# Optimization experiments

Hardware: AMD Instinct MI355X
Metric: run time of the kernel (lower is better)

The kernel has to match this reference:

```python
import jax, jax.numpy as jnp
import numpy as np

B, T, V = 32, 64, 30000
EMB, H, E, A = 512, 512, 256, 256


def setup_inputs() -> dict:
    key = jax.random.key(0)
    ks = jax.random.split(key, 16)
    s = lambda k, shape, fan: jax.random.normal(k, shape, jnp.float32) / np.sqrt(fan)
    return {
        "encoder_out": jax.random.normal(ks[0], (B, E), jnp.float32),
        "captions": jax.random.randint(ks[1], (B, T), 0, V),
        # attention params
        "We": s(ks[2], (A, E), E), "be": jnp.zeros((A,), jnp.float32),
        "Wd": s(ks[3], (A, H), H), "bd": jnp.zeros((A,), jnp.float32),
        "Wf": s(ks[4], (1, A), A), "bf": jnp.zeros((1,), jnp.float32),
        # embedding table
        "emb_table": s(ks[5], (V, EMB), 1.0),
        # LSTMCell params (PyTorch gate order i,f,g,o)
        "W_ih": s(ks[6], (4 * H, EMB + E), EMB + E),
        "W_hh": s(ks[7], (4 * H, H), H),
        "b_ih": jnp.zeros((4 * H,), jnp.float32),
        "b_hh": jnp.zeros((4 * H,), jnp.float32),
        # output projection
        "W_fc": s(ks[8], (V, H), H), "b_fc": jnp.zeros((V,), jnp.float32),
    }


def reference(encoder_out, captions, We, be, Wd, bd, Wf, bf, emb_table,
              W_ih, W_hh, b_ih, b_hh, W_fc, b_fc):
    # dropout layers are identity (eval mode)
    emb = emb_table[captions]                      # [B, T, EMB]
    att1 = encoder_out @ We.T + be                 # [B, A]  (encoder term, loop-invariant)

    def step(carry, e_t):
        h, c = carry
        # additive attention over a length-1 sequence -> alpha == 1
        att2 = h @ Wd.T + bd                       # [B, A]
        att = jnp.tanh(att1 + att2) @ Wf.T + bf    # [B, 1]
        alpha = jax.nn.softmax(att, axis=1)        # ones, kept for faithfulness
        context = encoder_out * alpha              # [B, E]
        x = jnp.concatenate([e_t, context], axis=1)  # [B, EMB+E]
        gates = x @ W_ih.T + b_ih + h @ W_hh.T + b_hh  # [B, 4H]
        i, f, g, o = jnp.split(gates, 4, axis=1)
        c_new = jax.nn.sigmoid(f) * c + jax.nn.sigmoid(i) * jnp.tanh(g)
        h_new = jax.nn.sigmoid(o) * jnp.tanh(c_new)
        out_t = h_new @ W_fc.T + b_fc              # [B, V]
        return (h_new, c_new), out_t

    h0 = jnp.zeros((encoder_out.shape[0], H), encoder_out.dtype)
    c0 = jnp.zeros_like(h0)
    _, outs = jax.lax.scan(step, (h0, c0), jnp.swapaxes(emb, 0, 1))  # [T, B, V]
    return jnp.swapaxes(outs, 0, 1)                                  # [B, T, V]
```

## Files before the change

### kernel.cpp

```cpp
#include <hip/hip_runtime.h>
#include <hip/hip_bf16.h>


#define BATCH 32
#define TT 64
#define VV 30000
#define HH 512
#define G4 2048
#define KX 768
#define RNN_WG 16
#define CONS_WG 240
#define NTILE 235

typedef __bf16 bf16x8 __attribute__((ext_vector_type(8)));
typedef float f32x4 __attribute__((ext_vector_type(4)));
typedef unsigned long long u64;

#define MFMA(a, b, c) __builtin_amdgcn_mfma_f32_16x16x32_bf16((a), (b), (c), 0, 0, 0)

__device__ __forceinline__ float sigf(float x) {
    return 1.0f / (1.0f + __expf(-x));
}
__device__ __forceinline__ float tanh_fast(float x) {
    return 1.0f - 2.0f / (__expf(2.0f * x) + 1.0f);
}
__device__ __forceinline__ bf16x8 cvt8(const float* __restrict__ p) {
    const f32x4 a = *(const f32x4*)p;
    const f32x4 b = *(const f32x4*)(p + 4);
    bf16x8 r;
    r[0] = (__bf16)a[0]; r[1] = (__bf16)a[1]; r[2] = (__bf16)a[2]; r[3] = (__bf16)a[3];
    r[4] = (__bf16)b[0]; r[5] = (__bf16)b[1]; r[6] = (__bf16)b[2]; r[7] = (__bf16)b[3];
    return r;
}

__global__ __launch_bounds__(256) void pre_kernel(
    const float* __restrict__ enc, const int* __restrict__ captions,
    const float* __restrict__ emb, const float* __restrict__ Wih,
    const float* __restrict__ bih, const float* __restrict__ bhh,
    float* __restrict__ pre) {
    __shared__ __bf16 aT[128 * 32];
    __shared__ __bf16 bT[128 * 32];
    __shared__ int capm[128];

    const int tid = threadIdx.x;
    const int nt = blockIdx.x;
    const int mt = blockIdx.y;

    if (tid < 128) {
        int m = mt * 128 + tid;
        capm[tid] = captions[(m & 31) * TT + (m >> 5)];
    }

    const int lane = tid & 63, wv = tid >> 6;
    const int ln = lane & 15, quad = lane >> 4;
    const int wm = wv & 1, wn = wv >> 1;

    f32x4 acc[4][4] = {};
    __syncthreads();

    for (int kc = 0; kc < 24; ++kc) {
        const int k0 = kc * 32;
        for (int i = tid; i < 512; i += 256) {
            int r = i >> 2, seg = i & 3;
            const float* src;
            if (k0 < 512) {
                src = emb + (size_t)capm[r] * 512 + k0 + seg * 8;
            } else {
                int b = (mt * 128 + r) & 31;
                src = enc + b * 256 + (k0 - 512) + seg * 8;
            }
            *(bf16x8*)&aT[r * 32 + seg * 8] = cvt8(src);
            *(bf16x8*)&bT[r * 32 + seg * 8] =
                cvt8(&Wih[(size_t)(nt * 128 + r) * KX + k0 + seg * 8]);
        }
        __syncthreads();
        bf16x8 af[4], bfr[4];
        for (int x = 0; x < 4; ++x) {
            af[x]  = *(const bf16x8*)&aT[(wm * 64 + x * 16 + ln) * 32 + quad * 8];
            bfr[x] = *(const bf16x8*)&bT[(wn * 64 + x * 16 + ln) * 32 + quad * 8];
        }
        for (int mi = 0; mi < 4; ++mi)
            for (int ni = 0; ni < 4; ++ni)
                acc[mi][ni] = MFMA(af[mi], bfr[ni], acc[mi][ni]);
        __syncthreads();
    }

    for (int ni = 0; ni < 4; ++ni) {
        int g = nt * 128 + wn * 64 + ni * 16 + ln;
        float bias = bih[g] + bhh[g];
        for (int mi = 0; mi < 4; ++mi) {
            int m = mt * 128 + wm * 64 + mi * 16 + quad * 4;
            int t = m >> 5, b = m & 31;
            f32x4 v = acc[mi][ni];
            v[0] += bias; v[1] += bias; v[2] += bias; v[3] += bias;
            *(f32x4*)&pre[((size_t)t * G4 + g) * BATCH + b] = v;
        }
    }
}

__global__ __launch_bounds__(256, 1) void fused_kernel(
    const float* __restrict__ pre, const float* __restrict__ Whh,
    __bf16* __restrict__ Hall, unsigned* __restrict__ flags,
    const float* __restrict__ Wfc, const float* __restrict__ bfc,
    float* __restrict__ out, int consume) {
    __shared__ char smem[131072];
    const int tid = threadIdx.x;
    const int lane = tid & 63, wv = tid >> 6;
    const int ln = lane & 15, quad = lane >> 4;

    if (blockIdx.x >= RNN_WG) {
        if (!consume) return;
        __bf16* aT = (__bf16*)smem;
        __bf16* bT = (__bf16*)(smem + 8192);
        const int wm = wv & 1, wn = wv >> 1;
        const int cw = blockIdx.x - RNN_WG;

        for (int j = cw; j < 16 * NTILE; j += CONS_WG) {
            const int mt = j / NTILE, nt = j % NTILE;
            if (tid < RNN_WG) {
                const unsigned fidx = (unsigned)(mt * 4 + 3) * RNN_WG + tid;
                while (__hip_atomic_load(&flags[fidx], __ATOMIC_RELAXED,
                                         __HIP_MEMORY_SCOPE_AGENT) == 0)
                    __builtin_amdgcn_s_sleep(2);
            }
            __syncthreads();

            f32x4 acc[4][4] = {};
            const size_t aBase = (size_t)mt * 128 * HH;
            for (int kc = 0; kc < 16; ++kc) {
                const int k0 = kc * 32;
                for (int i = tid; i < 512; i += 256) {
                    int r = i >> 2, seg = i & 3;
                    *(bf16x8*)&aT[r * 32 + seg * 8] = *(const bf16x8*)
                        &Hall[aBase + (size_t)r * HH + k0 + seg * 8];
                    int gr = nt * 128 + r;
                    if (gr >= VV) gr = VV - 1;
                    *(bf16x8*)&bT[r * 32 + seg * 8] =
                        cvt8(&Wfc[(size_t)gr * HH + k0 + seg * 8]);
                }
                __syncthreads();
                bf16x8 af[4], bfr[4];
                for (int x = 0; x < 4; ++x) {
                    af[x]  = *(const bf16x8*)&aT[(wm * 64 + x * 16 + ln) * 32 + quad * 8];
                    bfr[x] = *(const bf16x8*)&bT[(wn * 64 + x * 16 + ln) * 32 + quad * 8];
                }
                for (int mi = 0; mi < 4; ++mi)
                    for (int ni = 0; ni < 4; ++ni)
                        acc[mi][ni] = MFMA(af[mi], bfr[ni], acc[mi][ni]);
                __syncthreads();
            }

            for (int ni = 0; ni < 4; ++ni) {
                int n = nt * 128 + wn * 64 + ni * 16 + ln;
                if (n >= VV) continue;
                float bias = bfc[n];
                for (int mi = 0; mi < 4; ++mi) {
                    int m = mt * 128 + wm * 64 + mi * 16 + quad * 4;
                    for (int r = 0; r < 4; ++r) {
                        int mm = m + r, t = mm >> 5, b = mm & 31;
                        out[((size_t)b * TT + t) * VV + n] = acc[mi][ni][r] + bias;
                    }
                }
            }
        }
        return;
    }

    __bf16* whh = (__bf16*)smem;
    float*  gst = (float*)smem;
    const int w = blockIdx.x;

    for (int i = tid; i < 128 * 64; i += 256) {
        int r = i >> 6, k = (i & 63) << 3;
        int g = (r >> 5) * 512 + w * 32 + (r & 31);
        *(bf16x8*)&whh[r * 512 + k] = cvt8(&Whh[(size_t)g * HH + k]);
    }
    __syncthreads();

    bf16x8 bfrag[2][16];
#pragma unroll
    for (int nj = 0; nj < 2; ++nj)
#pragma unroll
        for (int kc = 0; kc < 16; ++kc)
            bfrag[nj][kc] = *(const bf16x8*)
                &whh[(wv * 32 + nj * 16 + ln) * 512 + kc * 32 + quad * 8];
    __syncthreads();

    const int b_pw = tid & 31;
    const int nl = tid >> 5;
    const int b0 = quad * 4;
    const size_t preg0 = (size_t)(wv * 512 + w * 32 + ln);
    float c[4] = {0.f, 0.f, 0.f, 0.f};

    f32x4 pr[2][2];
#pragma unroll
    for (int mi = 0; mi < 2; ++mi)
#pragma unroll
        for (int nj = 0; nj < 2; ++nj)
            pr[mi][nj] = *(const f32x4*)
                &pre[(preg0 + nj * 16) * BATCH + mi * 16 + b0];

    for (int t = 0; t < TT; ++t) {
        f32x4 acc[2][2];
#pragma unroll
        for (int mi = 0; mi < 2; ++mi)
#pragma unroll
            for (int nj = 0; nj < 2; ++nj)
                acc[mi][nj] = pr[mi][nj];

        if (t + 1 < TT) {
#pragma unroll
            for (int mi = 0; mi < 2; ++mi)
#pragma unroll
                for (int nj = 0; nj < 2; ++nj)
                    pr[mi][nj] = *(const f32x4*)
                        &pre[((size_t)(t + 1) * G4 + preg0 + nj * 16) * BATCH +
                             mi * 16 + b0];
        }

        if (t > 0) {
            if (tid < RNN_WG) {
                while (__hip_atomic_load(&flags[(t - 1) * RNN_WG + tid],
                                         __ATOMIC_RELAXED,
                                         __HIP_MEMORY_SCOPE_AGENT) == 0) {}
            }
        }
        __syncthreads();

        if (t > 0) {
            const __bf16* hbase = Hall + (size_t)(t - 1) * BATCH * HH;
            bf16x8 a[2][8];
#pragma unroll
            for (int half = 0; half < 2; ++half) {
#pragma unroll
                for (int mi = 0; mi < 2; ++mi)
#pragma unroll
                    for (int kk = 0; kk < 8; ++kk)
                        a[mi][kk] = *(const bf16x8*)
                            &hbase[(size_t)(mi * 16 + ln) * HH +
                                   (half * 8 + kk) * 32 + quad * 8];
#pragma unroll
                for (int kk = 0; kk < 8; ++kk)
#pragma unroll
                    for (int mi = 0; mi < 2; ++mi)
#pragma unroll
                        for (int nj = 0; nj < 2; ++nj)
                            acc[mi][nj] = MFMA(a[mi][kk],
                                               bfrag[nj][half * 8 + kk],
                                               acc[mi][nj]);
            }
        }
#pragma unroll
        for (int mi = 0; mi < 2; ++mi)
#pragma unroll
            for (int nj = 0; nj < 2; ++nj)
                *(f32x4*)&gst[(wv * 32 + nj * 16 + ln) * 36 + mi * 16 + b0] =
                    acc[mi][nj];
        __syncthreads();

        union { u64 u; __bf16 h4[4]; } pk;
#pragma unroll
        for (int j = 0; j < 4; ++j) {
            int cl = nl * 4 + j;
            float gi = gst[(cl)      * 36 + b_pw];
            float gf = gst[(32 + cl) * 36 + b_pw];
            float gg = gst[(64 + cl) * 36 + b_pw];
            float go = gst[(96 + cl) * 36 + b_pw];
            c[j] = sigf(gf) * c[j] + sigf(gi) * tanh_fast(gg);
            pk.h4[j] = (__bf16)(sigf(go) * tanh_fast(c[j]));
        }
        __hip_atomic_store(
            (u64*)&Hall[((size_t)t * BATCH + b_pw) * HH + w * 32 + nl * 4],
            pk.u, __ATOMIC_RELAXED, __HIP_MEMORY_SCOPE_AGENT);

        __syncthreads();
        if (tid == 0)
            __hip_atomic_store(&flags[t * RNN_WG + w], 1u, __ATOMIC_RELAXED,
                               __HIP_MEMORY_SCOPE_AGENT);
    }
}

__global__ __launch_bounds__(256) void out_kernel(
    const __bf16* __restrict__ Hall, const float* __restrict__ Wfc,
    const float* __restrict__ bfc, float* __restrict__ out) {
    __shared__ __bf16 aT[128 * 32];
    __shared__ __bf16 bT[128 * 32];

    const int tid = threadIdx.x;
    const int mt = blockIdx.x;
    const int nt = blockIdx.y;
    const int lane = tid & 63, wv = tid >> 6;
    const int ln = lane & 15, quad = lane >> 4;
    const int wm = wv & 1, wn = wv >> 1;

    f32x4 acc[4][4] = {};
    const size_t aBase = (size_t)mt * 128 * HH;

    for (int kc = 0; kc < 16; ++kc) {
        const int k0 = kc * 32;
        for (int i = tid; i < 512; i += 256) {
            int r = i >> 2, seg = i & 3;
            *(bf16x8*)&aT[r * 32 + seg * 8] =
                *(const bf16x8*)&Hall[aBase + (size_t)r * HH + k0 + seg * 8];
            int gr = nt * 128 + r;
            if (gr >= VV) gr = VV - 1;
            *(bf16x8*)&bT[r * 32 + seg * 8] =
                cvt8(&Wfc[(size_t)gr * HH + k0 + seg * 8]);
        }
        __syncthreads();
        bf16x8 af[4], bfr[4];
        for (int x = 0; x < 4; ++x) {
            af[x]  = *(const bf16x8*)&aT[(wm * 64 + x * 16 + ln) * 32 + quad * 8];
            bfr[x] = *(const bf16x8*)&bT[(wn * 64 + x * 16 + ln) * 32 + quad * 8];
        }
        for (int mi = 0; mi < 4; ++mi)
            for (int ni = 0; ni < 4; ++ni)
                acc[mi][ni] = MFMA(af[mi], bfr[ni], acc[mi][ni]);
        __syncthreads();
    }

    for (int ni = 0; ni < 4; ++ni) {
        int n = nt * 128 + wn * 64 + ni * 16 + ln;
        if (n >= VV) continue;
        float bias = bfc[n];
        for (int mi = 0; mi < 4; ++mi) {
            int m = mt * 128 + wm * 64 + mi * 16 + quad * 4;
            for (int r = 0; r < 4; ++r) {
                int mm = m + r, t = mm >> 5, b = mm & 31;
                out[((size_t)b * TT + t) * VV + n] = acc[mi][ni][r] + bias;
            }
        }
    }
}

extern "C" void kernel_launch(void* const* d_in, const int* in_sizes, int n_in,
                              void* d_out, int out_size, void* d_ws, size_t ws_size,
                              hipStream_t stream) {
    const float* enc      = (const float*)d_in[0];
    const int*   captions = (const int*)d_in[1];
    const float* emb      = (const float*)d_in[8];
    const float* Wih      = (const float*)d_in[9];
    const float* Whh      = (const float*)d_in[10];
    const float* bih      = (const float*)d_in[11];
    const float* bhh      = (const float*)d_in[12];
    const float* Wfc      = (const float*)d_in[13];
    const float* bfc      = (const float*)d_in[14];
    float* out = (float*)d_out;

    uint8_t* w = (uint8_t*)d_ws;
    unsigned* flags = (unsigned*)w;
    __bf16* Hall = (__bf16*)(w + 16384);
    const size_t PRE_OFF   = 16384 + (size_t)TT * BATCH * HH * 2;
    const size_t PRE_BYTES = (size_t)TT * G4 * BATCH * 4;
    const bool fused = ws_size >= PRE_OFF + PRE_BYTES;

    float* pre = fused ? (float*)(w + PRE_OFF) : (float*)d_out;

    hipMemsetAsync(flags, 0, 16384, stream);

    pre_kernel<<<dim3(16, 16), 256, 0, stream>>>(enc, captions, emb, Wih, bih, bhh, pre);
    fused_kernel<<<dim3(256), 256, 0, stream>>>(pre, Whh, Hall, flags, Wfc, bfc,
                                                out, fused ? 1 : 0);
    if (!fused)
        out_kernel<<<dim3(16, 235), 256, 0, stream>>>(Hall, Wfc, bfc, out);
}
```

Before: 868.8 us.

## Fold input-gate precompute into fused kernel with per-timestep-chunk readiness counters

The separate pre_kernel launch that computes x@W_ih for all timesteps is removed when the workspace is large enough. Its 256 tiles are now computed by the consumer workgroups of the fused kernel before they start the output projection. The recurrent workgroups wait on per-chunk counters (one chunk covers four timesteps), so the recurrence can start once the first chunk is ready instead of after the whole precompute. This removes one launch boundary and overlaps the precompute with the serial LSTM, at the cost of atomic stores and spin-waits.

```diff
diff --git a/kernel.cpp b/kernel.cpp
--- a/kernel.cpp
+++ b/kernel.cpp
@@ -99,21 +99,85 @@
 }
 
 __global__ __launch_bounds__(256, 1) void fused_kernel(
-    const float* __restrict__ pre, const float* __restrict__ Whh,
+    const float* __restrict__ enc, const int* __restrict__ captions,
+    const float* __restrict__ emb, const float* __restrict__ Wih,
+    const float* __restrict__ bih, const float* __restrict__ bhh,
+    float* __restrict__ pre, const float* __restrict__ Whh,
     __bf16* __restrict__ Hall, unsigned* __restrict__ flags,
+    unsigned* __restrict__ preCtr,
     const float* __restrict__ Wfc, const float* __restrict__ bfc,
-    float* __restrict__ out, int consume) {
+    float* __restrict__ out, int fused) {
     __shared__ char smem[131072];
     const int tid = threadIdx.x;
     const int lane = tid & 63, wv = tid >> 6;
     const int ln = lane & 15, quad = lane >> 4;
 
     if (blockIdx.x >= RNN_WG) {
-        if (!consume) return;
+        if (!fused) return;
         __bf16* aT = (__bf16*)smem;
         __bf16* bT = (__bf16*)(smem + 8192);
+        int* capm  = (int*)(smem + 16384);
         const int wm = wv & 1, wn = wv >> 1;
         const int cw = blockIdx.x - RNN_WG;
+
+        for (int j = cw; j < 256; j += CONS_WG) {
+            const int mtp = j >> 4, ntp = j & 15;
+            if (tid < 128) {
+                int m = mtp * 128 + tid;
+                capm[tid] = captions[(m & 31) * TT + (m >> 5)];
+            }
+            f32x4 acc[4][4] = {};
+            __syncthreads();
+
+            for (int kc = 0; kc < 24; ++kc) {
+                const int k0 = kc * 32;
+                for (int i = tid; i < 512; i += 256) {
+                    int r = i >> 2, seg = i & 3;
+                    const float* src;
+                    if (k0 < 512) {
+                        src = emb + (size_t)capm[r] * 512 + k0 + seg * 8;
+                    } else {
+                        int b = (mtp * 128 + r) & 31;
+                        src = enc + b * 256 + (k0 - 512) + seg * 8;
+                    }
+                    *(bf16x8*)&aT[r * 32 + seg * 8] = cvt8(src);
+                    *(bf16x8*)&bT[r * 32 + seg * 8] =
+                        cvt8(&Wih[(size_t)(ntp * 128 + r) * KX + k0 + seg * 8]);
+                }
+                __syncthreads();
+                bf16x8 af[4], bfr[4];
+                for (int x = 0; x < 4; ++x) {
+                    af[x]  = *(const bf16x8*)&aT[(wm * 64 + x * 16 + ln) * 32 + quad * 8];
+                    bfr[x] = *(const bf16x8*)&bT[(wn * 64 + x * 16 + ln) * 32 + quad * 8];
+                }
+                for (int mi = 0; mi < 4; ++mi)
+                    for (int ni = 0; ni < 4; ++ni)
+                        acc[mi][ni] = MFMA(af[mi], bfr[ni], acc[mi][ni]);
+                __syncthreads();
+            }
+
+            for (int ni = 0; ni < 4; ++ni) {
+                int g = ntp * 128 + wn * 64 + ni * 16 + ln;
+                float bias = bih[g] + bhh[g];
+                for (int mi = 0; mi < 4; ++mi) {
+                    int m = mtp * 128 + wm * 64 + mi * 16 + quad * 4;
+                    int t = m >> 5, b = m & 31;
+                    union { f32x4 v; u64 q[2]; } uu;
+                    uu.v = acc[mi][ni];
+                    uu.v[0] += bias; uu.v[1] += bias;
+                    uu.v[2] += bias; uu.v[3] += bias;
+                    u64* dst = (u64*)&pre[((size_t)t * G4 + g) * BATCH + b];
+                    __hip_atomic_store(dst, uu.q[0], __ATOMIC_RELAXED,
+                                       __HIP_MEMORY_SCOPE_AGENT);
+                    __hip_atomic_store(dst + 1, uu.q[1], __ATOMIC_RELAXED,
+                                       __HIP_MEMORY_SCOPE_AGENT);
+                }
+            }
+            __syncthreads();
+            if (tid == 0)
+                __hip_atomic_fetch_add(&preCtr[mtp], 1u, __ATOMIC_RELAXED,
+                                       __HIP_MEMORY_SCOPE_AGENT);
+        }
 
         for (int j = cw; j < 16 * NTILE; j += CONS_WG) {
             const int mt = j / NTILE, nt = j % NTILE;
@@ -191,6 +255,15 @@
     const int b0 = quad * 4;
     const size_t preg0 = (size_t)(wv * 512 + w * 32 + ln);
     float c[4] = {0.f, 0.f, 0.f, 0.f};
+    unsigned doneMask = 1u;
+
+    if (fused) {
+        if (tid == 0) {
+            while (__hip_atomic_load(&preCtr[0], __ATOMIC_RELAXED,
+                                     __HIP_MEMORY_SCOPE_AGENT) < 16u) {}
+        }
+        __syncthreads();
+    }
 
     f32x4 pr[2][2];
 #pragma unroll
@@ -209,6 +282,12 @@
                 acc[mi][nj] = pr[mi][nj];
 
         if (t + 1 < TT) {
+            const int mt2 = (t + 1) >> 2;
+            if (fused && !(doneMask & (1u << mt2))) {
+                while (__hip_atomic_load(&preCtr[mt2], __ATOMIC_ACQUIRE,
+                                         __HIP_MEMORY_SCOPE_AGENT) < 16u) {}
+                doneMask |= 1u << mt2;
+            }
 #pragma unroll
             for (int mi = 0; mi < 2; ++mi)
 #pragma unroll
@@ -348,7 +427,8 @@
     float* out = (float*)d_out;
 
     uint8_t* w = (uint8_t*)d_ws;
-    unsigned* flags = (unsigned*)w;
+    unsigned* flags  = (unsigned*)w;
+    unsigned* preCtr = (unsigned*)(w + 4096);
     __bf16* Hall = (__bf16*)(w + 16384);
     const size_t PRE_OFF   = 16384 + (size_t)TT * BATCH * HH * 2;
     const size_t PRE_BYTES = (size_t)TT * G4 * BATCH * 4;
@@ -358,9 +438,13 @@
 
     hipMemsetAsync(flags, 0, 16384, stream);
 
-    pre_kernel<<<dim3(16, 16), 256, 0, stream>>>(enc, captions, emb, Wih, bih, bhh, pre);
-    fused_kernel<<<dim3(256), 256, 0, stream>>>(pre, Whh, Hall, flags, Wfc, bfc,
-                                                out, fused ? 1 : 0);
+    if (!fused)
+        pre_kernel<<<dim3(16, 16), 256, 0, stream>>>(enc, captions, emb, Wih,
+                                                     bih, bhh, pre);
+    fused_kernel<<<dim3(256), 256, 0, stream>>>(enc, captions, emb, Wih, bih,
+                                                bhh, pre, Whh, Hall, flags,
+                                                preCtr, Wfc, bfc, out,
+                                                fused ? 1 : 0);
     if (!fused)
         out_kernel<<<dim3(16, 235), 256, 0, stream>>>(Hall, Wfc, bfc, out);
 }
```

Result: no change. 864.3 us (-0.5%).
